# Kernel optimization log

Measured on AMD Instinct MI355X. Metric: run time of the kernel, lower is better.

The kernel has to match this reference:

```python
import jax, jax.numpy as jnp
import numpy as np

B, C, N, S = 4, 64, 16384, 16
DIM_OUT = 64
SCALE = DIM_OUT ** (-0.5)


def setup_inputs() -> dict:
    key = jax.random.key(0)
    ks = jax.random.split(key, 8)
    return {
        "xyz": jax.random.normal(ks[0], (B, 3, N), dtype=jnp.float32),
        "neighbor_xyz": jax.random.normal(ks[1], (B, 3, N, S), dtype=jnp.float32),
        "points": jax.random.normal(ks[2], (B, C, N), dtype=jnp.float32),
        "neighbor_points": jax.random.normal(ks[3], (B, C, N, S), dtype=jnp.float32),
        "Wk": jax.random.normal(ks[4], (C, C), dtype=jnp.float32) * 0.05,
        "Wv": jax.random.normal(ks[5], (DIM_OUT, C + 3), dtype=jnp.float32) * 0.05,
        "Wp": jax.random.normal(ks[6], (C, 4), dtype=jnp.float32) * 0.05,
        "bp": jax.random.normal(ks[7], (C,), dtype=jnp.float32) * 0.05,
    }


def reference(xyz, neighbor_xyz, points, neighbor_points, Wk, Wv, Wp, bp):
    # relative position of each neighbor: [B,3,N,S]
    tmp = xyz[:, :, :, None] - neighbor_xyz
    xyz_norm = jnp.sqrt(jnp.sum(tmp * tmp, axis=1, keepdims=True))  # [B,1,N,S]
    pos = jnp.concatenate([tmp, xyz_norm], axis=1)  # [B,4,N,S]

    # 1x1 convs == per-point channel matmuls
    pos_enc = jnp.einsum('oc,bcns->bons', Wp, pos) + bp[None, :, None, None]
    k = jnp.einsum('oc,bcns->bons', Wk, neighbor_points + pos_enc)  # [B,C,N,S]
    v_in = jnp.concatenate([neighbor_points, tmp], axis=1)  # [B,C+3,N,S]
    v = jnp.einsum('oc,bcns->bons', Wv, v_in)  # [B,dim_out,N,S]

    q = points * SCALE  # [B,C,N]
    attn = jax.nn.softmax(jnp.einsum('bcn,bcns->bns', q, k), axis=-1)  # [B,N,S]
    out = jnp.einsum('bns,bcns->bcn', attn, v)  # [B,dim_out,N]
    return out
```

## Files before the change

kernel.cpp:

```cpp
#include <hip/hip_runtime.h>
#include <math.h>

constexpr int Nn = 16384;
constexpr int ST = 68;
constexpr size_t NS = (size_t)Nn * 16;

template <int CTRL>
__device__ __forceinline__ float dpp_f(float x) {
    return __int_as_float(
        __builtin_amdgcn_update_dpp(0, __float_as_int(x), CTRL, 0xF, 0xF, false));
}
__device__ __forceinline__ float qsum4(float v) {
    v += dpp_f<0xB1>(v);
    v += dpp_f<0x4E>(v);
    return v;
}
__device__ __forceinline__ float qmax4(float v) {
    v = fmaxf(v, dpp_f<0xB1>(v));
    v = fmaxf(v, dpp_f<0x4E>(v));
    return v;
}

__global__ __launch_bounds__(256, 4) void qkpp_kernel(
    const float* __restrict__ points, const float* __restrict__ Wk,
    const float* __restrict__ Wp, float* __restrict__ ws)
{
    const int tid = threadIdx.x;
    const int lane = tid & 63;
    const int q = lane >> 4;
    const int pt = blockIdx.x * 64 + (tid >> 6) * 16 + (lane & 15);
    const int b = pt >> 14;
    const int n = pt & (Nn - 1);

    float qk[16];
#pragma unroll
    for (int k = 0; k < 16; ++k) qk[k] = 0.f;

    const float* prow = points + (size_t)b * 64 * Nn + n;
    const float* wkq = Wk + 16 * q;
#pragma unroll 4
    for (int c = 0; c < 64; ++c) {
        const float qv = prow[(size_t)c * Nn];
        const float4 w0 = *(const float4*)(wkq + c * 64 + 0);
        const float4 w1 = *(const float4*)(wkq + c * 64 + 4);
        const float4 w2 = *(const float4*)(wkq + c * 64 + 8);
        const float4 w3 = *(const float4*)(wkq + c * 64 + 12);
        qk[0]  = fmaf(qv, w0.x, qk[0]);  qk[1]  = fmaf(qv, w0.y, qk[1]);
        qk[2]  = fmaf(qv, w0.z, qk[2]);  qk[3]  = fmaf(qv, w0.w, qk[3]);
        qk[4]  = fmaf(qv, w1.x, qk[4]);  qk[5]  = fmaf(qv, w1.y, qk[5]);
        qk[6]  = fmaf(qv, w1.z, qk[6]);  qk[7]  = fmaf(qv, w1.w, qk[7]);
        qk[8]  = fmaf(qv, w2.x, qk[8]);  qk[9]  = fmaf(qv, w2.y, qk[9]);
        qk[10] = fmaf(qv, w2.z, qk[10]); qk[11] = fmaf(qv, w2.w, qk[11]);
        qk[12] = fmaf(qv, w3.x, qk[12]); qk[13] = fmaf(qv, w3.y, qk[13]);
        qk[14] = fmaf(qv, w3.z, qk[14]); qk[15] = fmaf(qv, w3.w, qk[15]);
    }
#pragma unroll
    for (int k = 0; k < 16; ++k) qk[k] *= 0.125f;

    float p0 = 0.f, p1 = 0.f, p2 = 0.f, p3 = 0.f;
#pragma unroll
    for (int k = 0; k < 16; ++k) {
        const float4 wp4 = *(const float4*)(Wp + (16 * q + k) * 4);
        p0 = fmaf(qk[k], wp4.x, p0);
        p1 = fmaf(qk[k], wp4.y, p1);
        p2 = fmaf(qk[k], wp4.z, p2);
        p3 = fmaf(qk[k], wp4.w, p3);
    }
    p0 += __shfl_xor(p0, 16); p0 += __shfl_xor(p0, 32);
    p1 += __shfl_xor(p1, 16); p1 += __shfl_xor(p1, 32);
    p2 += __shfl_xor(p2, 16); p2 += __shfl_xor(p2, 32);
    p3 += __shfl_xor(p3, 16); p3 += __shfl_xor(p3, 32);

    float* orow = ws + (size_t)pt * ST + 16 * q;
    ((float4*)orow)[0] = make_float4(qk[0],  qk[1],  qk[2],  qk[3]);
    ((float4*)orow)[1] = make_float4(qk[4],  qk[5],  qk[6],  qk[7]);
    ((float4*)orow)[2] = make_float4(qk[8],  qk[9],  qk[10], qk[11]);
    ((float4*)orow)[3] = make_float4(qk[12], qk[13], qk[14], qk[15]);
    if (q == 0)
        *(float4*)(ws + (size_t)pt * ST + 64) = make_float4(p0, p1, p2, p3);
}

__global__ __launch_bounds__(256, 4) void attn_out_kernel(
    const float* __restrict__ xyz, const float* __restrict__ nxyz,
    const float* __restrict__ npts, const float* __restrict__ Wv,
    const float* __restrict__ ws, float* __restrict__ out)
{
    __shared__ float wvT[67 * 68];
    __shared__ __align__(16) float lexch[4][64][4];
    __shared__ float vbexch[67 * 17];

    const int tid = threadIdx.x;
    const int w = tid >> 6;
    const int l = tid & 63;
    const int p = l >> 2;
    const int sq = l & 3;
    const int gpt0 = blockIdx.x * 16;
    const int b = gpt0 >> 14;
    const int ng = gpt0 & (Nn - 1);

    const float* npb = npts + ((size_t)(b * 64 + 16 * w)) * NS + (size_t)ng * 16 + 4 * l;
    float4 npv4[16];
#pragma unroll
    for (int k = 0; k < 16; ++k) npv4[k] = *(const float4*)(npb + (size_t)k * NS);

    const float* qrow = ws + (size_t)(gpt0 + p) * ST + 16 * w;
    const float4 qqa = ((const float4*)qrow)[0];
    const float4 qqb = ((const float4*)qrow)[1];
    const float4 qqc = ((const float4*)qrow)[2];
    const float4 qqd = ((const float4*)qrow)[3];

    float4 d04, d14, d24, dn4, pp4;
    if (w == 3) {
        const float4 nx0 = *(const float4*)(nxyz + ((size_t)(b * 3 + 0) * Nn + ng) * 16 + 4 * l);
        const float4 nx1 = *(const float4*)(nxyz + ((size_t)(b * 3 + 1) * Nn + ng) * 16 + 4 * l);
        const float4 nx2 = *(const float4*)(nxyz + ((size_t)(b * 3 + 2) * Nn + ng) * 16 + 4 * l);
        const float x0 = xyz[(size_t)(b * 3 + 0) * Nn + ng + p];
        const float x1 = xyz[(size_t)(b * 3 + 1) * Nn + ng + p];
        const float x2 = xyz[(size_t)(b * 3 + 2) * Nn + ng + p];
        d04 = make_float4(x0 - nx0.x, x0 - nx0.y, x0 - nx0.z, x0 - nx0.w);
        d14 = make_float4(x1 - nx1.x, x1 - nx1.y, x1 - nx1.z, x1 - nx1.w);
        d24 = make_float4(x2 - nx2.x, x2 - nx2.y, x2 - nx2.z, x2 - nx2.w);
        dn4 = make_float4(sqrtf(d04.x * d04.x + d14.x * d14.x + d24.x * d24.x),
                          sqrtf(d04.y * d04.y + d14.y * d14.y + d24.y * d24.y),
                          sqrtf(d04.z * d04.z + d14.z * d14.z + d24.z * d24.z),
                          sqrtf(d04.w * d04.w + d14.w * d14.w + d24.w * d24.w));
        pp4 = *(const float4*)(ws + (size_t)(gpt0 + p) * ST + 64);
    }

    for (int idx = tid; idx < 64 * 67; idx += 256) {
        const int o = idx / 67, c = idx - o * 67;
        wvT[c * 68 + o] = Wv[idx];
    }

    const float qks[16] = {qqa.x, qqa.y, qqa.z, qqa.w, qqb.x, qqb.y, qqb.z, qqb.w,
                           qqc.x, qqc.y, qqc.z, qqc.w, qqd.x, qqd.y, qqd.z, qqd.w};
    float4 lp = make_float4(0.f, 0.f, 0.f, 0.f);
#pragma unroll
    for (int k = 0; k < 16; ++k) {
        lp.x = fmaf(qks[k], npv4[k].x, lp.x);
        lp.y = fmaf(qks[k], npv4[k].y, lp.y);
        lp.z = fmaf(qks[k], npv4[k].z, lp.z);
        lp.w = fmaf(qks[k], npv4[k].w, lp.w);
    }
    if (w == 3) {
        lp.x += pp4.x * d04.x + pp4.y * d14.x + pp4.z * d24.x + pp4.w * dn4.x;
        lp.y += pp4.x * d04.y + pp4.y * d14.y + pp4.z * d24.y + pp4.w * dn4.y;
        lp.z += pp4.x * d04.z + pp4.y * d14.z + pp4.z * d24.z + pp4.w * dn4.z;
        lp.w += pp4.x * d04.w + pp4.y * d14.w + pp4.z * d24.w + pp4.w * dn4.w;
    }

    __syncthreads();
    *(float4*)&lexch[w][l][0] = lp;
    __syncthreads();
    const float4 g0 = *(const float4*)&lexch[0][l][0];
    const float4 g1 = *(const float4*)&lexch[1][l][0];
    const float4 g2 = *(const float4*)&lexch[2][l][0];
    const float4 g3 = *(const float4*)&lexch[3][l][0];
    const float4 lg = make_float4(g0.x + g1.x + g2.x + g3.x,
                                  g0.y + g1.y + g2.y + g3.y,
                                  g0.z + g1.z + g2.z + g3.z,
                                  g0.w + g1.w + g2.w + g3.w);

    float mx = fmaxf(fmaxf(lg.x, lg.y), fmaxf(lg.z, lg.w));
    mx = qmax4(mx);
    const float e0 = __expf(lg.x - mx), e1 = __expf(lg.y - mx);
    const float e2 = __expf(lg.z - mx), e3 = __expf(lg.w - mx);
    const float se = qsum4((e0 + e1) + (e2 + e3));
    const float inv = 1.0f / se;
    const float at0 = e0 * inv, at1 = e1 * inv, at2 = e2 * inv, at3 = e3 * inv;

#pragma unroll
    for (int k = 0; k < 16; ++k) {
        float v = at0 * npv4[k].x + at1 * npv4[k].y + at2 * npv4[k].z + at3 * npv4[k].w;
        v = qsum4(v);
        if (sq == (k & 3)) vbexch[(16 * w + k) * 17 + p] = v;
    }
    if (w == 3) {
        const float t0 = qsum4(at0 * d04.x + at1 * d04.y + at2 * d04.z + at3 * d04.w);
        const float t1 = qsum4(at0 * d14.x + at1 * d14.y + at2 * d14.z + at3 * d14.w);
        const float t2 = qsum4(at0 * d24.x + at1 * d24.y + at2 * d24.z + at3 * d24.w);
        if (sq == 0) vbexch[64 * 17 + p] = t0;
        else if (sq == 1) vbexch[65 * 17 + p] = t1;
        else if (sq == 2) vbexch[66 * 17 + p] = t2;
    }
    __syncthreads();

    float4 oa = make_float4(0.f, 0.f, 0.f, 0.f);
#pragma unroll
    for (int c = 0; c < 67; ++c) {
        const float vb = vbexch[c * 17 + p];
        const float4 wq = *(const float4*)&wvT[c * 68 + 16 * w + 4 * sq];
        oa.x = fmaf(vb, wq.x, oa.x);
        oa.y = fmaf(vb, wq.y, oa.y);
        oa.z = fmaf(vb, wq.z, oa.z);
        oa.w = fmaf(vb, wq.w, oa.w);
    }

    float* ob = out + ((size_t)(b * 64 + 16 * w + 4 * sq)) * Nn + ng + p;
    ob[0]              = oa.x;
    ob[(size_t)Nn]     = oa.y;
    ob[(size_t)Nn * 2] = oa.z;
    ob[(size_t)Nn * 3] = oa.w;
}

extern "C" void kernel_launch(void* const* d_in, const int* in_sizes, int n_in,
                              void* d_out, int out_size, void* d_ws, size_t ws_size,
                              hipStream_t stream) {
    const float* xyz    = (const float*)d_in[0];
    const float* nxyz   = (const float*)d_in[1];
    const float* points = (const float*)d_in[2];
    const float* npts   = (const float*)d_in[3];
    const float* Wk     = (const float*)d_in[4];
    const float* Wv     = (const float*)d_in[5];
    const float* Wp     = (const float*)d_in[6];
    float* out = (float*)d_out;
    float* ws = (float*)d_ws;

    hipLaunchKernelGGL(qkpp_kernel,     dim3(1024), dim3(256), 0, stream,
                       points, Wk, Wp, ws);
    hipLaunchKernelGGL(attn_out_kernel, dim3(4096), dim3(256), 0, stream,
                       xyz, nxyz, npts, Wv, ws, out);
}
```

Measured before the change: 117.9 us.

## Make attention kernel persistent over 8 groups with register double-buffered prefetch

Each block of the attention/output kernel now handles 8 groups of 16 points instead of one. It loads the transposed Wv into shared memory once per block and double-buffers the neighbor-feature loads for the next group in registers while computing the current one. Plain __syncthreads is replaced by a lighter barrier that waits only on LDS counters, so outstanding global prefetches are not drained at each sync. The costs are roughly doubled register pressure (launch bounds lowered to 2), only 512 blocks in the grid, and less occupancy-based latency hiding.

Result: slower. 129.5 us (+9.8%).

```diff
diff --git a/kernel.cpp b/kernel.cpp
--- a/kernel.cpp
+++ b/kernel.cpp
@@ -4,6 +4,7 @@
 constexpr int Nn = 16384;
 constexpr int ST = 68;
 constexpr size_t NS = (size_t)Nn * 16;
+constexpr int GPB = 8;
 
 template <int CTRL>
 __device__ __forceinline__ float dpp_f(float x) {
@@ -20,6 +21,9 @@
     v = fmaxf(v, dpp_f<0x4E>(v));
     return v;
 }
+
+#define BAR() do { asm volatile("s_waitcnt lgkmcnt(0)" ::: "memory"); \
+    __builtin_amdgcn_s_barrier(); asm volatile("" ::: "memory"); } while (0)
 
 __global__ __launch_bounds__(256, 4) void qkpp_kernel(
     const float* __restrict__ points, const float* __restrict__ Wk,
@@ -80,7 +84,7 @@
         *(float4*)(ws + (size_t)pt * ST + 64) = make_float4(p0, p1, p2, p3);
 }
 
-__global__ __launch_bounds__(256, 4) void attn_out_kernel(
+__global__ __launch_bounds__(256, 2) void attn_out_kernel(
     const float* __restrict__ xyz, const float* __restrict__ nxyz,
     const float* __restrict__ npts, const float* __restrict__ Wv,
     const float* __restrict__ ws, float* __restrict__ out)
@@ -94,113 +98,141 @@
     const int l = tid & 63;
     const int p = l >> 2;
     const int sq = l & 3;
-    const int gpt0 = blockIdx.x * 16;
-    const int b = gpt0 >> 14;
-    const int ng = gpt0 & (Nn - 1);
-
-    const float* npb = npts + ((size_t)(b * 64 + 16 * w)) * NS + (size_t)ng * 16 + 4 * l;
-    float4 npv4[16];
-#pragma unroll
-    for (int k = 0; k < 16; ++k) npv4[k] = *(const float4*)(npb + (size_t)k * NS);
-
-    const float* qrow = ws + (size_t)(gpt0 + p) * ST + 16 * w;
-    const float4 qqa = ((const float4*)qrow)[0];
-    const float4 qqb = ((const float4*)qrow)[1];
-    const float4 qqc = ((const float4*)qrow)[2];
-    const float4 qqd = ((const float4*)qrow)[3];
-
-    float4 d04, d14, d24, dn4, pp4;
-    if (w == 3) {
-        const float4 nx0 = *(const float4*)(nxyz + ((size_t)(b * 3 + 0) * Nn + ng) * 16 + 4 * l);
-        const float4 nx1 = *(const float4*)(nxyz + ((size_t)(b * 3 + 1) * Nn + ng) * 16 + 4 * l);
-        const float4 nx2 = *(const float4*)(nxyz + ((size_t)(b * 3 + 2) * Nn + ng) * 16 + 4 * l);
-        const float x0 = xyz[(size_t)(b * 3 + 0) * Nn + ng + p];
-        const float x1 = xyz[(size_t)(b * 3 + 1) * Nn + ng + p];
-        const float x2 = xyz[(size_t)(b * 3 + 2) * Nn + ng + p];
-        d04 = make_float4(x0 - nx0.x, x0 - nx0.y, x0 - nx0.z, x0 - nx0.w);
-        d14 = make_float4(x1 - nx1.x, x1 - nx1.y, x1 - nx1.z, x1 - nx1.w);
-        d24 = make_float4(x2 - nx2.x, x2 - nx2.y, x2 - nx2.z, x2 - nx2.w);
-        dn4 = make_float4(sqrtf(d04.x * d04.x + d14.x * d14.x + d24.x * d24.x),
-                          sqrtf(d04.y * d04.y + d14.y * d14.y + d24.y * d24.y),
-                          sqrtf(d04.z * d04.z + d14.z * d14.z + d24.z * d24.z),
-                          sqrtf(d04.w * d04.w + d14.w * d14.w + d24.w * d24.w));
-        pp4 = *(const float4*)(ws + (size_t)(gpt0 + p) * ST + 64);
-    }
+
+    const int gptbase = blockIdx.x * (16 * GPB);
+    const int b = gptbase >> 14;
+    const int ngbase = gptbase & (Nn - 1);
 
     for (int idx = tid; idx < 64 * 67; idx += 256) {
         const int o = idx / 67, c = idx - o * 67;
         wvT[c * 68 + o] = Wv[idx];
     }
 
-    const float qks[16] = {qqa.x, qqa.y, qqa.z, qqa.w, qqb.x, qqb.y, qqb.z, qqb.w,
-                           qqc.x, qqc.y, qqc.z, qqc.w, qqd.x, qqd.y, qqd.z, qqd.w};
-    float4 lp = make_float4(0.f, 0.f, 0.f, 0.f);
-#pragma unroll
-    for (int k = 0; k < 16; ++k) {
-        lp.x = fmaf(qks[k], npv4[k].x, lp.x);
-        lp.y = fmaf(qks[k], npv4[k].y, lp.y);
-        lp.z = fmaf(qks[k], npv4[k].z, lp.z);
-        lp.w = fmaf(qks[k], npv4[k].w, lp.w);
-    }
-    if (w == 3) {
-        lp.x += pp4.x * d04.x + pp4.y * d14.x + pp4.z * d24.x + pp4.w * dn4.x;
-        lp.y += pp4.x * d04.y + pp4.y * d14.y + pp4.z * d24.y + pp4.w * dn4.y;
-        lp.z += pp4.x * d04.z + pp4.y * d14.z + pp4.z * d24.z + pp4.w * dn4.z;
-        lp.w += pp4.x * d04.w + pp4.y * d14.w + pp4.z * d24.w + pp4.w * dn4.w;
-    }
-
-    __syncthreads();
-    *(float4*)&lexch[w][l][0] = lp;
-    __syncthreads();
-    const float4 g0 = *(const float4*)&lexch[0][l][0];
-    const float4 g1 = *(const float4*)&lexch[1][l][0];
-    const float4 g2 = *(const float4*)&lexch[2][l][0];
-    const float4 g3 = *(const float4*)&lexch[3][l][0];
-    const float4 lg = make_float4(g0.x + g1.x + g2.x + g3.x,
-                                  g0.y + g1.y + g2.y + g3.y,
-                                  g0.z + g1.z + g2.z + g3.z,
-                                  g0.w + g1.w + g2.w + g3.w);
-
-    float mx = fmaxf(fmaxf(lg.x, lg.y), fmaxf(lg.z, lg.w));
-    mx = qmax4(mx);
-    const float e0 = __expf(lg.x - mx), e1 = __expf(lg.y - mx);
-    const float e2 = __expf(lg.z - mx), e3 = __expf(lg.w - mx);
-    const float se = qsum4((e0 + e1) + (e2 + e3));
-    const float inv = 1.0f / se;
-    const float at0 = e0 * inv, at1 = e1 * inv, at2 = e2 * inv, at3 = e3 * inv;
-
-#pragma unroll
-    for (int k = 0; k < 16; ++k) {
-        float v = at0 * npv4[k].x + at1 * npv4[k].y + at2 * npv4[k].z + at3 * npv4[k].w;
-        v = qsum4(v);
-        if (sq == (k & 3)) vbexch[(16 * w + k) * 17 + p] = v;
-    }
-    if (w == 3) {
-        const float t0 = qsum4(at0 * d04.x + at1 * d04.y + at2 * d04.z + at3 * d04.w);
-        const float t1 = qsum4(at0 * d14.x + at1 * d14.y + at2 * d14.z + at3 * d14.w);
-        const float t2 = qsum4(at0 * d24.x + at1 * d24.y + at2 * d24.z + at3 * d24.w);
-        if (sq == 0) vbexch[64 * 17 + p] = t0;
-        else if (sq == 1) vbexch[65 * 17 + p] = t1;
-        else if (sq == 2) vbexch[66 * 17 + p] = t2;
-    }
-    __syncthreads();
-
-    float4 oa = make_float4(0.f, 0.f, 0.f, 0.f);
-#pragma unroll
-    for (int c = 0; c < 67; ++c) {
-        const float vb = vbexch[c * 17 + p];
-        const float4 wq = *(const float4*)&wvT[c * 68 + 16 * w + 4 * sq];
-        oa.x = fmaf(vb, wq.x, oa.x);
-        oa.y = fmaf(vb, wq.y, oa.y);
-        oa.z = fmaf(vb, wq.z, oa.z);
-        oa.w = fmaf(vb, wq.w, oa.w);
-    }
-
-    float* ob = out + ((size_t)(b * 64 + 16 * w + 4 * sq)) * Nn + ng + p;
-    ob[0]              = oa.x;
-    ob[(size_t)Nn]     = oa.y;
-    ob[(size_t)Nn * 2] = oa.z;
-    ob[(size_t)Nn * 3] = oa.w;
+    const float* npb0 = npts + ((size_t)(b * 64 + 16 * w)) * NS + (size_t)ngbase * 16 + 4 * l;
+
+    float4 npA[16], npB[16], qqA[4], qqB[4], nxA[3], nxB[3];
+    float4 ppA = make_float4(0,0,0,0), ppB = make_float4(0,0,0,0);
+    float xA[3] = {0,0,0}, xB[3] = {0,0,0};
+
+    auto prefetch = [&](int g, float4 (&np)[16], float4 (&qq)[4],
+                        float4 (&nx)[3], float (&xx)[3], float4& pp) {
+        const float* npb = npb0 + (size_t)g * 256;
+#pragma unroll
+        for (int k = 0; k < 16; ++k) np[k] = *(const float4*)(npb + (size_t)k * NS);
+        const float* qrow = ws + (size_t)(gptbase + 16 * g + p) * ST + 16 * w;
+        qq[0] = ((const float4*)qrow)[0];
+        qq[1] = ((const float4*)qrow)[1];
+        qq[2] = ((const float4*)qrow)[2];
+        qq[3] = ((const float4*)qrow)[3];
+        if (w == 3) {
+            const int ng = ngbase + 16 * g;
+            nx[0] = *(const float4*)(nxyz + ((size_t)(b * 3 + 0) * Nn + ng) * 16 + 4 * l);
+            nx[1] = *(const float4*)(nxyz + ((size_t)(b * 3 + 1) * Nn + ng) * 16 + 4 * l);
+            nx[2] = *(const float4*)(nxyz + ((size_t)(b * 3 + 2) * Nn + ng) * 16 + 4 * l);
+            xx[0] = xyz[(size_t)(b * 3 + 0) * Nn + ng + p];
+            xx[1] = xyz[(size_t)(b * 3 + 1) * Nn + ng + p];
+            xx[2] = xyz[(size_t)(b * 3 + 2) * Nn + ng + p];
+            pp = *(const float4*)(ws + (size_t)(gptbase + 16 * g + p) * ST + 64);
+        }
+    };
+
+    auto step = [&](int g, float4 (&np)[16], float4 (&qq)[4],
+                    float4 (&nx)[3], float (&xx)[3], float4& pp) {
+        const int ng = ngbase + 16 * g;
+
+        float4 d04 = make_float4(0,0,0,0), d14 = d04, d24 = d04, dn4 = d04;
+        if (w == 3) {
+            d04 = make_float4(xx[0] - nx[0].x, xx[0] - nx[0].y, xx[0] - nx[0].z, xx[0] - nx[0].w);
+            d14 = make_float4(xx[1] - nx[1].x, xx[1] - nx[1].y, xx[1] - nx[1].z, xx[1] - nx[1].w);
+            d24 = make_float4(xx[2] - nx[2].x, xx[2] - nx[2].y, xx[2] - nx[2].z, xx[2] - nx[2].w);
+            dn4 = make_float4(sqrtf(d04.x * d04.x + d14.x * d14.x + d24.x * d24.x),
+                              sqrtf(d04.y * d04.y + d14.y * d14.y + d24.y * d24.y),
+                              sqrtf(d04.z * d04.z + d14.z * d14.z + d24.z * d24.z),
+                              sqrtf(d04.w * d04.w + d14.w * d14.w + d24.w * d24.w));
+        }
+
+        const float qks[16] = {qq[0].x, qq[0].y, qq[0].z, qq[0].w,
+                               qq[1].x, qq[1].y, qq[1].z, qq[1].w,
+                               qq[2].x, qq[2].y, qq[2].z, qq[2].w,
+                               qq[3].x, qq[3].y, qq[3].z, qq[3].w};
+        float4 lp = make_float4(0.f, 0.f, 0.f, 0.f);
+#pragma unroll
+        for (int k = 0; k < 16; ++k) {
+            lp.x = fmaf(qks[k], np[k].x, lp.x);
+            lp.y = fmaf(qks[k], np[k].y, lp.y);
+            lp.z = fmaf(qks[k], np[k].z, lp.z);
+            lp.w = fmaf(qks[k], np[k].w, lp.w);
+        }
+        if (w == 3) {
+            lp.x += pp.x * d04.x + pp.y * d14.x + pp.z * d24.x + pp.w * dn4.x;
+            lp.y += pp.x * d04.y + pp.y * d14.y + pp.z * d24.y + pp.w * dn4.y;
+            lp.z += pp.x * d04.z + pp.y * d14.z + pp.z * d24.z + pp.w * dn4.z;
+            lp.w += pp.x * d04.w + pp.y * d14.w + pp.z * d24.w + pp.w * dn4.w;
+        }
+
+        BAR();
+        *(float4*)&lexch[w][l][0] = lp;
+        BAR();
+        const float4 g0 = *(const float4*)&lexch[0][l][0];
+        const float4 g1 = *(const float4*)&lexch[1][l][0];
+        const float4 g2 = *(const float4*)&lexch[2][l][0];
+        const float4 g3 = *(const float4*)&lexch[3][l][0];
+        const float4 lg = make_float4(g0.x + g1.x + g2.x + g3.x,
+                                      g0.y + g1.y + g2.y + g3.y,
+                                      g0.z + g1.z + g2.z + g3.z,
+                                      g0.w + g1.w + g2.w + g3.w);
+
+        float mx = fmaxf(fmaxf(lg.x, lg.y), fmaxf(lg.z, lg.w));
+        mx = qmax4(mx);
+        const float e0 = __expf(lg.x - mx), e1 = __expf(lg.y - mx);
+        const float e2 = __expf(lg.z - mx), e3 = __expf(lg.w - mx);
+        const float se = qsum4((e0 + e1) + (e2 + e3));
+        const float inv = 1.0f / se;
+        const float at0 = e0 * inv, at1 = e1 * inv, at2 = e2 * inv, at3 = e3 * inv;
+
+#pragma unroll
+        for (int k = 0; k < 16; ++k) {
+            float v = at0 * np[k].x + at1 * np[k].y + at2 * np[k].z + at3 * np[k].w;
+            v = qsum4(v);
+            if (sq == (k & 3)) vbexch[(16 * w + k) * 17 + p] = v;
+        }
+        if (w == 3) {
+            const float t0 = qsum4(at0 * d04.x + at1 * d04.y + at2 * d04.z + at3 * d04.w);
+            const float t1 = qsum4(at0 * d14.x + at1 * d14.y + at2 * d14.z + at3 * d14.w);
+            const float t2 = qsum4(at0 * d24.x + at1 * d24.y + at2 * d24.z + at3 * d24.w);
+            if (sq == 0) vbexch[64 * 17 + p] = t0;
+            else if (sq == 1) vbexch[65 * 17 + p] = t1;
+            else if (sq == 2) vbexch[66 * 17 + p] = t2;
+        }
+        BAR();
+
+        float4 oa = make_float4(0.f, 0.f, 0.f, 0.f);
+#pragma unroll
+        for (int c = 0; c < 67; ++c) {
+            const float vb = vbexch[c * 17 + p];
+            const float4 wq = *(const float4*)&wvT[c * 68 + 16 * w + 4 * sq];
+            oa.x = fmaf(vb, wq.x, oa.x);
+            oa.y = fmaf(vb, wq.y, oa.y);
+            oa.z = fmaf(vb, wq.z, oa.z);
+            oa.w = fmaf(vb, wq.w, oa.w);
+        }
+
+        float* ob = out + ((size_t)(b * 64 + 16 * w + 4 * sq)) * Nn + ng + p;
+        ob[0]              = oa.x;
+        ob[(size_t)Nn]     = oa.y;
+        ob[(size_t)Nn * 2] = oa.z;
+        ob[(size_t)Nn * 3] = oa.w;
+    };
+
+    prefetch(0, npA, qqA, nxA, xA, ppA);
+#pragma unroll 1
+    for (int gg = 0; gg < GPB / 2; ++gg) {
+        prefetch(2 * gg + 1, npB, qqB, nxB, xB, ppB);
+        step(2 * gg, npA, qqA, nxA, xA, ppA);
+        if (2 * gg + 2 < GPB)
+            prefetch(2 * gg + 2, npA, qqA, nxA, xA, ppA);
+        step(2 * gg + 1, npB, qqB, nxB, xB, ppB);
+    }
 }
 
 extern "C" void kernel_launch(void* const* d_in, const int* in_sizes, int n_in,
@@ -218,6 +250,6 @@
 
     hipLaunchKernelGGL(qkpp_kernel,     dim3(1024), dim3(256), 0, stream,
                        points, Wk, Wp, ws);
-    hipLaunchKernelGGL(attn_out_kernel, dim3(4096), dim3(256), 0, stream,
+    hipLaunchKernelGGL(attn_out_kernel, dim3(512),  dim3(256), 0, stream,
                        xyz, nxyz, npts, Wv, ws, out);
 }
```
